# Kernel optimization log

Hardware: AMD Instinct MI355X
Metric: run time of the kernel (lower is better)

The kernel has to match this reference:

```python
import jax, jax.numpy as jnp
import numpy as np

B, N, S = 256, 512, 32
D_ENT, D_KEY, D_IN, D_FUNC, D_TYPE, H = 256, 32, 1024, 256, 259, 32


def _init_linear(k, out_d, in_d):
    kw, kb = jax.random.split(k)
    bound = 1.0 / np.sqrt(in_d)
    W = jax.random.uniform(kw, (out_d, in_d), minval=-bound, maxval=bound, dtype=jnp.float32)
    b = jax.random.uniform(kb, (out_d,), minval=-bound, maxval=bound, dtype=jnp.float32)
    return W, b


def setup_inputs() -> dict:
    key = jax.random.key(0)
    ks = jax.random.split(key, 16)
    inp = {
        "embedding": jax.random.normal(ks[0], (B, D_IN), jnp.float32),
        "available_unit_type_mask": (jax.random.uniform(ks[1], (B, D_TYPE)) < 0.5).astype(jnp.float32),
        "available_units_mask": jnp.ones((B, N), jnp.float32),
        "entity_embedding": jax.random.normal(ks[2], (B, N, D_ENT), jnp.float32),
        "selected_units": jax.random.randint(ks[3], (B, S), 0, N, dtype=jnp.int32),
        "end_embedding": jax.random.uniform(ks[4], (1, D_KEY), minval=-1.0, maxval=1.0, dtype=jnp.float32) / np.sqrt(D_KEY),
    }
    inp["W_key"], inp["b_key"] = _init_linear(ks[5], D_KEY, D_ENT)
    inp["W_func"], inp["b_func"] = _init_linear(ks[6], D_FUNC, D_TYPE)
    inp["W_fc1"], inp["b_fc1"] = _init_linear(ks[7], D_FUNC, D_IN)
    inp["W_fc2"], inp["b_fc2"] = _init_linear(ks[8], D_KEY, D_FUNC)
    inp["W_embed"], inp["b_embed"] = _init_linear(ks[9], D_IN, D_KEY)
    inp["W_ih"], inp["b_ih"] = _init_linear(ks[10], 4 * H, D_KEY)
    inp["W_hh"], inp["b_hh"] = _init_linear(ks[11], 4 * H, H)
    return inp


def reference(embedding, available_unit_type_mask, available_units_mask, entity_embedding,
              selected_units, end_embedding, W_key, b_key, W_func, b_func, W_fc1, b_fc1,
              W_fc2, b_fc2, W_embed, b_embed, W_ih, b_ih, W_hh, b_hh):
    Bv, Nv, _ = entity_embedding.shape
    Sv = selected_units.shape[1]
    # keys for each entity + end-flag embedding appended -> [B, N+1, key_dim]
    key_t = jnp.einsum('bnd,kd->bnk', entity_embedding, W_key) + b_key
    end = jnp.broadcast_to(end_embedding[None, :, :], (Bv, 1, end_embedding.shape[1]))
    pad_key = jnp.concatenate([key_t, end], axis=1)
    # mask: entities + end flag; teacher-forced selected positions forced to 1
    mask0 = jnp.concatenate([available_units_mask, jnp.ones((Bv, 1), available_units_mask.dtype)], axis=1)
    mask0 = mask0.at[jnp.arange(Bv)[:, None], selected_units].set(1.0)
    func_embed = jax.nn.relu(available_unit_type_mask @ W_func.T + b_func)
    inv_n = 1.0 / jnp.float32(Nv)  # split_entity_num = end_flag_index = num_units
    bidx = jnp.arange(Bv)
    # per-step selected index (dummy 0 on the final end-flag step) and validity
    sel_seq = jnp.concatenate([selected_units.T, jnp.zeros((1, Bv), selected_units.dtype)], axis=0)
    valid_seq = jnp.concatenate([jnp.ones((Sv, Bv), jnp.float32), jnp.zeros((1, Bv), jnp.float32)], axis=0)

    def step(carry, xs):
        emb, h, c, mask = carry
        sel, valid = xs
        # query = fc2(relu(fc1(emb) + func_embed))
        x = jax.nn.relu(emb @ W_fc1.T + b_fc1 + func_embed) @ W_fc2.T + b_fc2
        # one LSTM step
        gates = x @ W_ih.T + b_ih + h @ W_hh.T + b_hh
        i_g, f_g, g_g, o_g = jnp.split(gates, 4, axis=1)
        c = jax.nn.sigmoid(f_g) * c + jax.nn.sigmoid(i_g) * jnp.tanh(g_g)
        h = jax.nn.sigmoid(o_g) * jnp.tanh(c)
        # masked dot-product over keys -> logits [B, N+1]
        q = jnp.einsum('bk,bnk->bn', h, pad_key) - (1.0 - mask) * 1e9
        # mark selected unit unavailable for subsequent steps
        mask = mask.at[bidx, sel].set(jnp.where(valid > 0, 0.0, mask[bidx, sel]))
        # one-hot gather of selected key, averaged, fed back into embedding
        emb_sel = pad_key[bidx, sel] * inv_n
        emb = emb + (emb_sel @ W_embed.T + b_embed) * valid[:, None]
        return (emb, h, c, mask), q

    h0 = jnp.zeros((Bv, W_hh.shape[1]), jnp.float32)
    c0 = jnp.zeros_like(h0)
    (emb, _, _, _), logits = jax.lax.scan(step, (embedding, h0, c0, mask0), (sel_seq, valid_seq))
    logits = jnp.transpose(logits, (1, 0, 2))  # [B, S+1, N+1]
    return logits, emb
```

## Files before the change

### kernel.cpp

```cpp
#include <hip/hip_runtime.h>
#include <math.h>

#define BB_ 256
#define NN_ 512
#define SS_ 32
#define NP1 513
#define SP1 33
#define D_IN 1024
#define D_TYPE 259
#define INV_N (1.0f/512.0f)

typedef short s16x4 __attribute__((ext_vector_type(4)));
typedef short s16x8 __attribute__((ext_vector_type(8)));
typedef float f32x4 __attribute__((ext_vector_type(4)));

#if defined(__has_builtin)
#if __has_builtin(__builtin_amdgcn_rcpf)
#define FRCP(x) __builtin_amdgcn_rcpf(x)
#else
#define FRCP(x) (1.0f / (x))
#endif
#else
#define FRCP(x) (1.0f / (x))
#endif

__device__ __forceinline__ float fsig(float x) { return FRCP(1.0f + __expf(-x)); }
__device__ __forceinline__ float ftanh(float x) { return fmaf(-2.0f, FRCP(1.0f + __expf(2.0f * x)), 1.0f); }
__device__ __forceinline__ short f2bf(float f) {
    unsigned u = __float_as_uint(f);
    unsigned r = (u + 0x7FFFu + ((u >> 16) & 1u)) >> 16;
    return (short)r;
}
__device__ __forceinline__ float bf2f(short s) {
    unsigned u = ((unsigned)(unsigned short)s) << 16;
    return __uint_as_float(u);
}

__global__ __launch_bounds__(256) void front_kernel(
    const float* __restrict__ ent, const float* __restrict__ Wk,
    const float* __restrict__ bk, const float* __restrict__ endv,
    const float* __restrict__ Wemb, const float* __restrict__ bemb,
    const float* __restrict__ Wfc1, const float* __restrict__ emb0,
    const float* __restrict__ bfc1, const float* __restrict__ atm,
    const float* __restrict__ Wf, const float* __restrict__ bf,
    short* __restrict__ pkbf, float* __restrict__ WcombT,
    float* __restrict__ cbv, float* __restrict__ act_pre)
{
    __shared__ char u_raw[33280];
    short* a_st   = (short*)u_raw;
    float* wemb_s = (float*)(u_raw + 18688);
    float* a_lds  = (float*)u_raw;
    float* w_lds  = (float*)(u_raw + 16640);

    const int tid = threadIdx.x;
    const int bid = blockIdx.x;
    const int lane = tid & 63, w = tid >> 6;
    const int nl = lane & 15, q = lane >> 4;

    if (bid < 1024) {
        const size_t rowbase = (size_t)bid * 128;
        s16x8 bfr[8][2];
#pragma unroll
        for (int s = 0; s < 8; s++)
#pragma unroll
            for (int t = 0; t < 2; t++) {
                const float* src = Wk + (size_t)(t * 16 + nl) * 256 + s * 32 + q * 8;
                float4 v0 = *(const float4*)(src);
                float4 v1 = *(const float4*)(src + 4);
                s16x8 bv;
                bv[0] = f2bf(v0.x); bv[1] = f2bf(v0.y); bv[2] = f2bf(v0.z); bv[3] = f2bf(v0.w);
                bv[4] = f2bf(v1.x); bv[5] = f2bf(v1.y); bv[6] = f2bf(v1.z); bv[7] = f2bf(v1.w);
                bfr[s][t] = bv;
            }
        f32x4 acc[2][2];
#pragma unroll
        for (int mt = 0; mt < 2; mt++)
#pragma unroll
            for (int t = 0; t < 2; t++) acc[mt][t] = (f32x4)0.0f;

        for (int kc = 0; kc < 4; ++kc) {
            __syncthreads();
#pragma unroll
            for (int p = 0; p < 8; p++) {
                int flat = p * 256 + tid;
                int row = flat >> 4;
                int f4 = flat & 15;
                float4 v = *(const float4*)(ent + (rowbase + row) * 256 + kc * 64 + f4 * 4);
                s16x4 sv;
                sv[0] = f2bf(v.x); sv[1] = f2bf(v.y); sv[2] = f2bf(v.z); sv[3] = f2bf(v.w);
                *(s16x4*)&a_st[row * 72 + f4 * 4] = sv;
            }
            __syncthreads();
#pragma unroll
            for (int ks = 0; ks < 2; ks++) {
                const int sg = kc * 2 + ks;
#pragma unroll
                for (int mt = 0; mt < 2; mt++) {
                    s16x8 af = *(const s16x8*)&a_st[(w * 32 + mt * 16 + nl) * 72 + ks * 32 + q * 8];
#pragma unroll
                    for (int t = 0; t < 2; t++)
                        acc[mt][t] = __builtin_amdgcn_mfma_f32_16x16x32_bf16(af, bfr[sg][t], acc[mt][t], 0, 0, 0);
                }
            }
        }
        float bkv[2];
        bkv[0] = bk[nl]; bkv[1] = bk[16 + nl];
#pragma unroll
        for (int mt = 0; mt < 2; mt++)
#pragma unroll
            for (int t = 0; t < 2; t++)
#pragma unroll
                for (int r = 0; r < 4; r++) {
                    int rowg = (int)rowbase + w * 32 + mt * 16 + q * 4 + r;
                    int b = rowg >> 9, n = rowg & 511;
                    pkbf[((size_t)b * NP1 + n) * 32 + t * 16 + nl] = f2bf(acc[mt][t][r] + bkv[t]);
                }
    } else if (bid < 1026) {
        const int m0 = bid - 1024;
        f32x4 acc[2][3];
#pragma unroll
        for (int mt = 0; mt < 2; mt++)
#pragma unroll
            for (int t = 0; t < 3; t++) acc[mt][t] = (f32x4)0.0f;

        for (int kc = 0; kc < 16; ++kc) {
            __syncthreads();
#pragma unroll
            for (int p = 0; p < 8; p++) {
                int flat = p * 256 + tid;
                int row = flat >> 4;
                int f4 = flat & 15;
                float4 v = *(const float4*)(Wfc1 + (size_t)(m0 * 128 + row) * D_IN + kc * 64 + f4 * 4);
                s16x4 sv;
                sv[0] = f2bf(v.x); sv[1] = f2bf(v.y); sv[2] = f2bf(v.z); sv[3] = f2bf(v.w);
                *(s16x4*)&a_st[row * 72 + f4 * 4] = sv;
            }
            {
                int r = tid >> 2, c0 = tid & 3;
#pragma unroll
                for (int cc = 0; cc < 9; cc++) {
                    int col = c0 + cc * 4;
                    if (col < 33) {
                        float v = (col < 32) ? Wemb[(size_t)(kc * 64 + r) * 32 + col]
                                             : bemb[kc * 64 + r];
                        wemb_s[r * 33 + col] = v;
                    }
                }
            }
            __syncthreads();
#pragma unroll
            for (int ks = 0; ks < 2; ks++) {
                s16x8 bv[3];
#pragma unroll
                for (int t = 0; t < 3; t++) {
                    int n = t * 16 + nl;
#pragma unroll
                    for (int jj = 0; jj < 8; jj++) {
                        float v = (n < 33) ? wemb_s[(ks * 32 + q * 8 + jj) * 33 + n] : 0.0f;
                        bv[t][jj] = f2bf(v);
                    }
                }
#pragma unroll
                for (int mt = 0; mt < 2; mt++) {
                    s16x8 af = *(const s16x8*)&a_st[(w * 32 + mt * 16 + nl) * 72 + ks * 32 + q * 8];
#pragma unroll
                    for (int t = 0; t < 3; t++)
                        acc[mt][t] = __builtin_amdgcn_mfma_f32_16x16x32_bf16(af, bv[t], acc[mt][t], 0, 0, 0);
                }
            }
        }
#pragma unroll
        for (int mt = 0; mt < 2; mt++)
#pragma unroll
            for (int t = 0; t < 3; t++)
#pragma unroll
                for (int r = 0; r < 4; r++) {
                    int j = m0 * 128 + w * 32 + mt * 16 + q * 4 + r;
                    int n = t * 16 + nl;
                    if (n < 32) WcombT[j * 32 + n] = acc[mt][t][r];
                    else if (n == 32) cbv[j] = acc[mt][t][r];
                }
    } else if (bid == 1026) {
        const int k = tid & 31, b0 = tid >> 5;
        short evk = f2bf(endv[k]);
        for (int b = b0; b < BB_; b += 8)
            pkbf[((size_t)b * NP1 + 512) * 32 + k] = evk;
    } else {
        const int idx = bid - 1027;
        const int jt = idx & 15, bt = idx >> 4;
        const int bb = tid >> 4, jj = tid & 15;

#pragma unroll 4
        for (int r = 0; r < 16; r++) {
            a_lds[r * 260 + tid] = atm[(size_t)(bt * 16 + r) * D_TYPE + tid];
            w_lds[r * 260 + tid] = Wf[(size_t)(jt * 16 + r) * D_TYPE + tid];
            if (tid < 3) {
                a_lds[r * 260 + 256 + tid] = atm[(size_t)(bt * 16 + r) * D_TYPE + 256 + tid];
                w_lds[r * 260 + 256 + tid] = Wf[(size_t)(jt * 16 + r) * D_TYPE + 256 + tid];
            }
        }
        __syncthreads();
        float accf = 0.0f;
        {
            const float4* ap = (const float4*)&a_lds[bb * 260];
            const float4* wp = (const float4*)&w_lds[jj * 260];
#pragma unroll 8
            for (int i4 = 0; i4 < 64; i4++) {
                float4 a = ap[i4]; float4 wv = wp[i4];
                accf = fmaf(a.x, wv.x, accf); accf = fmaf(a.y, wv.y, accf);
                accf = fmaf(a.z, wv.z, accf); accf = fmaf(a.w, wv.w, accf);
            }
            for (int i = 256; i < 259; i++) accf = fmaf(a_lds[bb * 260 + i], w_lds[jj * 260 + i], accf);
        }
        float acc = 0.0f;
        for (int c = 0; c < 4; c++) {
            __syncthreads();
#pragma unroll
            for (int p = 0; p < 4; p++) {
                int l4 = p * 256 + tid;
                int r = l4 >> 6, k4 = l4 & 63;
                *(float4*)&a_lds[r * 260 + k4 * 4] =
                    *(const float4*)(emb0 + (size_t)(bt * 16 + r) * D_IN + c * 256 + k4 * 4);
                *(float4*)&w_lds[r * 260 + k4 * 4] =
                    *(const float4*)(Wfc1 + (size_t)(jt * 16 + r) * D_IN + c * 256 + k4 * 4);
            }
            __syncthreads();
#pragma unroll 8
            for (int k4 = 0; k4 < 64; k4++) {
                float4 a = *(const float4*)&a_lds[bb * 260 + k4 * 4];
                float4 wv = *(const float4*)&w_lds[jj * 260 + k4 * 4];
                acc = fmaf(a.x, wv.x, acc); acc = fmaf(a.y, wv.y, acc);
                acc = fmaf(a.z, wv.z, acc); acc = fmaf(a.w, wv.w, acc);
            }
        }
        const int b = bt * 16 + bb, j = jt * 16 + jj;
        act_pre[b * 256 + j] = acc + bfc1[j] + fmaxf(accf + bf[j], 0.0f);
    }
}

__global__ __launch_bounds__(256, 1) void back_kernel(
    const short* __restrict__ pkbf, const float* __restrict__ act_pre0,
    const int* __restrict__ sel, const float* __restrict__ avail,
    const float* __restrict__ Wfc2, const float* __restrict__ bfc2,
    const float* __restrict__ Wih, const float* __restrict__ bih,
    const float* __restrict__ bhh, const float* __restrict__ Whh,
    const float* __restrict__ WcombT, const float* __restrict__ cbv,
    const float* __restrict__ emb0, const float* __restrict__ Wemb,
    const float* __restrict__ bemb,
    float* __restrict__ logits, float* __restrict__ emb_out)
{
    __shared__ float S[19204];
    __shared__ int sel_l[SS_];
    float* rap_l  = S;
    float* red_l  = S + 8580;
    float* x_l    = S + 17028;
    float* cumE_l = S + 18084;
    float* ssel_l = S + 19140;
    float* xg_l   = S;
    float* h_all  = S + 4224;
    float* m0_l   = S + 8580;
    int*   tf_l   = (int*)(S + 9093);

    const int tid = threadIdx.x;
    const int b = blockIdx.x;
    const int lane = tid & 63, w = tid >> 6;
    const int nl = lane & 15, q = lane >> 4;

    if (tid < SS_) sel_l[tid] = sel[b * SS_ + tid];

    {
        const int k = tid & 31, sq = tid >> 5;
        const int sq4 = sq * 4;
        int s0 = sel[b * SS_ + sq4 + 0];
        int s1 = sel[b * SS_ + sq4 + 1];
        int s2 = sel[b * SS_ + sq4 + 2];
        int s3 = sel[b * SS_ + sq4 + 3];
        float v0 = bf2f(pkbf[((size_t)b * NP1 + s0) * 32 + k]) * INV_N;
        float v1 = bf2f(pkbf[((size_t)b * NP1 + s1) * 32 + k]) * INV_N;
        float v2 = bf2f(pkbf[((size_t)b * NP1 + s2) * 32 + k]) * INV_N;
        float v3 = bf2f(pkbf[((size_t)b * NP1 + s3) * 32 + k]) * INV_N;
        float p0 = v0, p1 = p0 + v1, p2 = p1 + v2, p3 = p2 + v3;
        x_l[sq * 32 + k] = p3;
        __syncthreads();
        float off = 0.0f;
        for (int p = 0; p < 8; p++) if (p < sq) off += x_l[p * 32 + k];
        cumE_l[(sq4 + 1) * 32 + k] = off + p0;
        cumE_l[(sq4 + 2) * 32 + k] = off + p1;
        cumE_l[(sq4 + 3) * 32 + k] = off + p2;
        cumE_l[(sq4 + 4) * 32 + k] = off + p3;
        if (tid < 32) cumE_l[tid] = 0.0f;
        if (sq == 7) ssel_l[k] = off + p3;
    }
    __syncthreads();

    {
        float wcr[32];
#pragma unroll
        for (int k4 = 0; k4 < 8; k4++) {
            float4 v = *(const float4*)(WcombT + (size_t)tid * 32 + k4 * 4);
            wcr[k4*4] = v.x; wcr[k4*4+1] = v.y; wcr[k4*4+2] = v.z; wcr[k4*4+3] = v.w;
        }
        const float cbr = cbv[tid];
        const float ap0v = act_pre0[b * 256 + tid];
        for (int t = 0; t < SP1; ++t) {
            float ap = fmaf((float)t, cbr, ap0v);
            const float4* ce = (const float4*)&cumE_l[t * 32];
#pragma unroll
            for (int k4 = 0; k4 < 8; k4++) {
                float4 e = ce[k4];
                ap = fmaf(e.x, wcr[k4*4], ap);   ap = fmaf(e.y, wcr[k4*4+1], ap);
                ap = fmaf(e.z, wcr[k4*4+2], ap); ap = fmaf(e.w, wcr[k4*4+3], ap);
            }
            rap_l[t * 260 + tid] = fmaxf(ap, 0.0f);
        }
    }
    __syncthreads();

    {
        const int seg = tid >> 5, i = tid & 31;
        float wfc2r[32];
#pragma unroll
        for (int i4 = 0; i4 < 8; i4++) {
            float4 v = *(const float4*)(Wfc2 + (size_t)i * 256 + seg * 32 + i4 * 4);
            wfc2r[i4*4] = v.x; wfc2r[i4*4+1] = v.y; wfc2r[i4*4+2] = v.z; wfc2r[i4*4+3] = v.w;
        }
        for (int t = 0; t < SP1; ++t) {
            float part = 0.0f;
            const float4* rp = (const float4*)&rap_l[t * 260 + seg * 32];
#pragma unroll
            for (int i4 = 0; i4 < 8; i4++) {
                float4 rv = rp[i4];
                part = fmaf(rv.x, wfc2r[i4*4], part);   part = fmaf(rv.y, wfc2r[i4*4+1], part);
                part = fmaf(rv.z, wfc2r[i4*4+2], part); part = fmaf(rv.w, wfc2r[i4*4+3], part);
            }
            red_l[t * 256 + seg * 32 + i] = part;
        }
    }
    __syncthreads();

    for (int p = 0; p < 5; p++) {
        int idx = p * 256 + tid;
        if (idx < SP1 * 32) {
            int t = idx >> 5, i = idx & 31;
            float x = bfc2[i];
#pragma unroll
            for (int s = 0; s < 8; s++) x += red_l[t * 256 + s * 32 + i];
            x_l[t * 32 + i] = x;
        }
    }
    __syncthreads();

    {
        const int g = tid & 127, half = tid >> 7;
        float wihr[32];
#pragma unroll
        for (int k4 = 0; k4 < 8; k4++) {
            float4 v = *(const float4*)(Wih + (size_t)g * 32 + k4 * 4);
            wihr[k4*4] = v.x; wihr[k4*4+1] = v.y; wihr[k4*4+2] = v.z; wihr[k4*4+3] = v.w;
        }
        const float bihg = bih[g] + bhh[g];
        for (int t = half; t < SP1; t += 2) {
            float gg = bihg;
            const float4* xp = (const float4*)&x_l[t * 32];
#pragma unroll
            for (int k4 = 0; k4 < 8; k4++) {
                float4 xv = xp[k4];
                gg = fmaf(xv.x, wihr[k4*4], gg);   gg = fmaf(xv.y, wihr[k4*4+1], gg);
                gg = fmaf(xv.z, wihr[k4*4+2], gg); gg = fmaf(xv.w, wihr[k4*4+3], gg);
            }
            xg_l[t * 128 + g] = gg;
        }
    }
    __syncthreads();

    if (tid < 64) {
        float whh0[32], whh1[32];
#pragma unroll
        for (int k4 = 0; k4 < 8; k4++) {
            float4 v0 = *(const float4*)(Whh + (size_t)tid * 32 + k4 * 4);
            float4 v1 = *(const float4*)(Whh + (size_t)(tid + 64) * 32 + k4 * 4);
            whh0[k4*4] = v0.x; whh0[k4*4+1] = v0.y; whh0[k4*4+2] = v0.z; whh0[k4*4+3] = v0.w;
            whh1[k4*4] = v1.x; whh1[k4*4+1] = v1.y; whh1[k4*4+2] = v1.z; whh1[k4*4+3] = v1.w;
        }
        float c = 0.0f, h = 0.0f;
        for (int t = 0; t < SP1; ++t) {
            float g0 = xg_l[t * 128 + tid];
            float g1 = xg_l[t * 128 + 64 + tid];
            if (t > 0) {
#pragma unroll
                for (int k = 0; k < 32; k++) {
                    float hk = __shfl(h, k);
                    g0 = fmaf(hk, whh0[k], g0);
                    g1 = fmaf(hk, whh1[k], g1);
                }
            }
            float og0 = __shfl_xor(g0, 32);
            float og1 = __shfl_xor(g1, 32);
            float ig = fsig(g0);
            float fg = fsig(og0);
            float gv = ftanh(g1);
            float og = fsig(og1);
            float cn = fg * c + ig * gv;
            float hn = og * ftanh(cn);
            if (tid < 32) {
                c = cn; h = hn;
                h_all[t * 32 + tid] = hn;
            }
        }
    } else {
        for (int n = tid - 64; n < NP1; n += 192) {
            float m = (n < NN_) ? avail[(size_t)b * NN_ + n] : 1.0f;
            int tf = 1000;
#pragma unroll 8
            for (int s = 0; s < SS_; s++) {
                int sv = sel_l[s];
                if (sv == n) { m = 1.0f; if (s < tf) tf = s; }
            }
            m0_l[n] = m; tf_l[n] = tf;
        }
    }
    __syncthreads();

    {
        s16x8 afr[3];
#pragma unroll
        for (int mt = 0; mt < 3; mt++) {
            int row = mt * 16 + nl;
            s16x8 av;
#pragma unroll
            for (int jj = 0; jj < 8; jj++) {
                float v = (row < SP1) ? h_all[row * 32 + q * 8 + jj] : 0.0f;
                av[jj] = f2bf(v);
            }
            afr[mt] = av;
        }
        for (int tt = w; tt < 33; tt += 4) {
            int n = tt * 16 + nl;
            bool nv = n < NP1;
            s16x8 bv = nv ? *(const s16x8*)(pkbf + ((size_t)b * NP1 + n) * 32 + q * 8) : (s16x8)0;
            f32x4 acc[3];
#pragma unroll
            for (int mt = 0; mt < 3; mt++)
                acc[mt] = __builtin_amdgcn_mfma_f32_16x16x32_bf16(afr[mt], bv, (f32x4)0.0f, 0, 0, 0);
            float m0v = nv ? m0_l[n] : 0.0f;
            int tfv = nv ? tf_l[n] : 0;
#pragma unroll
            for (int mt = 0; mt < 3; mt++)
#pragma unroll
                for (int r = 0; r < 4; r++) {
                    int t = mt * 16 + q * 4 + r;
                    if (t < SP1 && nv) {
                        float mv = (t <= tfv) ? m0v : 0.0f;
                        logits[((size_t)b * SP1 + t) * NP1 + n] = acc[mt][r] - (1.0f - mv) * 1e9f;
                    }
                }
        }
    }

#pragma unroll
    for (int p = 0; p < 4; p++) {
        int i = p * 256 + tid;
        float acc = emb0[(size_t)b * D_IN + i] + 32.0f * bemb[i];
        const float* wr = Wemb + (size_t)i * 32;
#pragma unroll
        for (int k4 = 0; k4 < 8; k4++) {
            float4 wv = *(const float4*)(wr + k4 * 4);
            acc = fmaf(ssel_l[k4*4+0], wv.x, acc);
            acc = fmaf(ssel_l[k4*4+1], wv.y, acc);
            acc = fmaf(ssel_l[k4*4+2], wv.z, acc);
            acc = fmaf(ssel_l[k4*4+3], wv.w, acc);
        }
        emb_out[(size_t)b * D_IN + i] = acc;
    }
}

extern "C" void kernel_launch(void* const* d_in, const int* in_sizes, int n_in,
                              void* d_out, int out_size, void* d_ws, size_t ws_size,
                              hipStream_t stream)
{
    (void)in_sizes; (void)n_in; (void)out_size; (void)ws_size;
    const float* embedding = (const float*)d_in[0];
    const float* atm       = (const float*)d_in[1];
    const float* avail     = (const float*)d_in[2];
    const float* ent       = (const float*)d_in[3];
    const int*   sel       = (const int*)  d_in[4];
    const float* endv      = (const float*)d_in[5];
    const float* Wk   = (const float*)d_in[6];
    const float* bk   = (const float*)d_in[7];
    const float* Wf   = (const float*)d_in[8];
    const float* bf   = (const float*)d_in[9];
    const float* Wfc1 = (const float*)d_in[10];
    const float* bfc1 = (const float*)d_in[11];
    const float* Wfc2 = (const float*)d_in[12];
    const float* bfc2 = (const float*)d_in[13];
    const float* Wemb = (const float*)d_in[14];
    const float* bemb = (const float*)d_in[15];
    const float* Wih  = (const float*)d_in[16];
    const float* bih  = (const float*)d_in[17];
    const float* Whh  = (const float*)d_in[18];
    const float* bhh  = (const float*)d_in[19];

    float* ws = (float*)d_ws;
    float* act_pre = ws;
    float* WcombT  = act_pre + BB_ * 256;
    float* cbv     = WcombT + 256 * 32;
    short* pkbf    = (short*)(cbv + 256);

    float* logits  = (float*)d_out;
    float* emb_out = logits + (size_t)BB_ * SP1 * NP1;

    front_kernel<<<1283, 256, 0, stream>>>(ent, Wk, bk, endv, Wemb, bemb,
                                           Wfc1, embedding, bfc1, atm, Wf, bf,
                                           pkbf, WcombT, cbv, act_pre);
    back_kernel<<<BB_, 256, 0, stream>>>(pkbf, act_pre, sel, avail,
                                         Wfc2, bfc2, Wih, bih, bhh, Whh,
                                         WcombT, cbv, embedding, Wemb, bemb,
                                         logits, emb_out);
}
```

Measured before the change: 310.6 us.

## Double-buffer entity key GEMM with async global-to-LDS loads and reorder block roles

The entity-key projection blocks now handle 64 rows each (2048 blocks) and stream fp32 entity tiles straight into LDS with global_load_lds in a double-buffered, XOR-swizzled layout, converting to bf16 at fragment-read time instead of on the store path. Block roles are reordered so the fc1/func-embed blocks and the Wcomb blocks come first in the grid, and the fp32 dot loops use four independent accumulators. The goal is to overlap global loads with MFMA work, spread the memory-bound key GEMM over more blocks, and start the long-running blocks early. In exchange it relies on hand-placed waitcnt/barrier sequencing, which is fragile, and it spends more LDS bandwidth reading fp32.

Result: faster. 298.9 us (-3.8%).

```diff
diff --git a/kernel.cpp b/kernel.cpp
--- a/kernel.cpp
+++ b/kernel.cpp
@@ -9,6 +9,13 @@
 #define D_IN 1024
 #define D_TYPE 259
 #define INV_N (1.0f/512.0f)
+
+#define N_ACT 256
+#define COMB_BASE 256
+#define END_BID 258
+#define KEY_BASE 259
+#define N_KEY 2048
+#define FRONT_GRID (KEY_BASE + N_KEY)
 
 typedef short s16x4 __attribute__((ext_vector_type(4)));
 typedef short s16x8 __attribute__((ext_vector_type(8)));
@@ -46,19 +53,39 @@
     short* __restrict__ pkbf, float* __restrict__ WcombT,
     float* __restrict__ cbv, float* __restrict__ act_pre)
 {
-    __shared__ char u_raw[33280];
+    __shared__ __align__(128) char u_raw[33280];
     short* a_st   = (short*)u_raw;
     float* wemb_s = (float*)(u_raw + 18688);
     float* a_lds  = (float*)u_raw;
     float* w_lds  = (float*)(u_raw + 16640);
+    float* kb     = (float*)u_raw;
 
     const int tid = threadIdx.x;
     const int bid = blockIdx.x;
     const int lane = tid & 63, w = tid >> 6;
     const int nl = lane & 15, q = lane >> 4;
 
-    if (bid < 1024) {
-        const size_t rowbase = (size_t)bid * 128;
+    if (bid >= KEY_BASE) {
+        const size_t rowbase = (size_t)(bid - KEY_BASE) * 64;
+
+#define KSTAGE(kc_, bi_) do {                                                     \
+        _Pragma("unroll")                                                         \
+        for (int p_ = 0; p_ < 4; p_++) {                                          \
+            int flat_ = p_ * 256 + tid;                                           \
+            int row_ = flat_ >> 4, u_ = flat_ & 15;                               \
+            int gf4_ = (u_ & 8) | ((u_ ^ row_) & 7);                              \
+            const float* src_ = ent + (((rowbase + (size_t)row_) << 8)            \
+                                       + (kc_) * 64 + gf4_ * 4);                  \
+            char* dst_ = u_raw + (bi_) * 16384 + ((p_ << 8) + (w << 6)) * 16;     \
+            __builtin_amdgcn_global_load_lds(                                     \
+                (const __attribute__((address_space(1))) void*)src_,              \
+                (__attribute__((address_space(3))) void*)dst_, 16, 0, 0);         \
+        }                                                                         \
+    } while (0)
+
+        KSTAGE(0, 0);
+        KSTAGE(1, 1);
+
         s16x8 bfr[8][2];
 #pragma unroll
         for (int s = 0; s < 8; s++)
@@ -72,51 +99,113 @@
                 bv[4] = f2bf(v1.x); bv[5] = f2bf(v1.y); bv[6] = f2bf(v1.z); bv[7] = f2bf(v1.w);
                 bfr[s][t] = bv;
             }
-        f32x4 acc[2][2];
-#pragma unroll
-        for (int mt = 0; mt < 2; mt++)
-#pragma unroll
-            for (int t = 0; t < 2; t++) acc[mt][t] = (f32x4)0.0f;
-
+
+        f32x4 acc[2];
+        acc[0] = (f32x4)0.0f; acc[1] = (f32x4)0.0f;
+
+        const int rl = w * 16 + nl;
+        const int rx = rl & 7;
+
+        asm volatile("s_waitcnt vmcnt(4)" ::: "memory");
+        __builtin_amdgcn_s_barrier();
+        asm volatile("" ::: "memory");
+
+#pragma unroll
         for (int kc = 0; kc < 4; ++kc) {
+            const float* kbc = kb + (kc & 1) * 4096;
+#pragma unroll
+            for (int ks = 0; ks < 2; ks++) {
+                int s0 = ks * 8 + ((q * 2) ^ rx);
+                int s1 = ks * 8 + ((q * 2 + 1) ^ rx);
+                f32x4 a0 = *(const f32x4*)&kbc[rl * 64 + s0 * 4];
+                f32x4 a1 = *(const f32x4*)&kbc[rl * 64 + s1 * 4];
+                s16x8 af;
+                af[0] = f2bf(a0[0]); af[1] = f2bf(a0[1]); af[2] = f2bf(a0[2]); af[3] = f2bf(a0[3]);
+                af[4] = f2bf(a1[0]); af[5] = f2bf(a1[1]); af[6] = f2bf(a1[2]); af[7] = f2bf(a1[3]);
+                acc[0] = __builtin_amdgcn_mfma_f32_16x16x32_bf16(af, bfr[kc * 2 + ks][0], acc[0], 0, 0, 0);
+                acc[1] = __builtin_amdgcn_mfma_f32_16x16x32_bf16(af, bfr[kc * 2 + ks][1], acc[1], 0, 0, 0);
+            }
+            if (kc < 2) {
+                asm volatile("s_waitcnt lgkmcnt(0)" ::: "memory");
+                __builtin_amdgcn_s_barrier();
+                asm volatile("" ::: "memory");
+                KSTAGE(kc + 2, kc & 1);
+                asm volatile("s_waitcnt vmcnt(4)" ::: "memory");
+                __builtin_amdgcn_s_barrier();
+                asm volatile("" ::: "memory");
+            } else if (kc == 2) {
+                asm volatile("s_waitcnt vmcnt(0)" ::: "memory");
+                __builtin_amdgcn_s_barrier();
+                asm volatile("" ::: "memory");
+            }
+        }
+#undef KSTAGE
+
+        float bkv0 = bk[nl], bkv1 = bk[16 + nl];
+#pragma unroll
+        for (int t = 0; t < 2; t++)
+#pragma unroll
+            for (int r = 0; r < 4; r++) {
+                int rowg = (int)rowbase + w * 16 + q * 4 + r;
+                int b = rowg >> 9, n = rowg & 511;
+                pkbf[((size_t)b * NP1 + n) * 32 + t * 16 + nl] =
+                    f2bf(acc[t][r] + (t ? bkv1 : bkv0));
+            }
+    } else if (bid < N_ACT) {
+        const int idx = bid;
+        const int jt = idx & 15, bt = idx >> 4;
+        const int bb = tid >> 4, jj = tid & 15;
+
+#pragma unroll 4
+        for (int r = 0; r < 16; r++) {
+            a_lds[r * 260 + tid] = atm[(size_t)(bt * 16 + r) * D_TYPE + tid];
+            w_lds[r * 260 + tid] = Wf[(size_t)(jt * 16 + r) * D_TYPE + tid];
+            if (tid < 3) {
+                a_lds[r * 260 + 256 + tid] = atm[(size_t)(bt * 16 + r) * D_TYPE + 256 + tid];
+                w_lds[r * 260 + 256 + tid] = Wf[(size_t)(jt * 16 + r) * D_TYPE + 256 + tid];
+            }
+        }
+        __syncthreads();
+        float accf;
+        {
+            float f0 = 0.0f, f1 = 0.0f, f2 = 0.0f, f3 = 0.0f;
+            const float4* ap = (const float4*)&a_lds[bb * 260];
+            const float4* wp = (const float4*)&w_lds[jj * 260];
+#pragma unroll 8
+            for (int i4 = 0; i4 < 64; i4++) {
+                float4 a = ap[i4]; float4 wv = wp[i4];
+                f0 = fmaf(a.x, wv.x, f0); f1 = fmaf(a.y, wv.y, f1);
+                f2 = fmaf(a.z, wv.z, f2); f3 = fmaf(a.w, wv.w, f3);
+            }
+            accf = (f0 + f1) + (f2 + f3);
+            for (int i = 256; i < 259; i++) accf = fmaf(a_lds[bb * 260 + i], w_lds[jj * 260 + i], accf);
+        }
+        float c0 = 0.0f, c1 = 0.0f, c2 = 0.0f, c3 = 0.0f;
+        for (int c = 0; c < 4; c++) {
             __syncthreads();
 #pragma unroll
-            for (int p = 0; p < 8; p++) {
-                int flat = p * 256 + tid;
-                int row = flat >> 4;
-                int f4 = flat & 15;
-                float4 v = *(const float4*)(ent + (rowbase + row) * 256 + kc * 64 + f4 * 4);
-                s16x4 sv;
-                sv[0] = f2bf(v.x); sv[1] = f2bf(v.y); sv[2] = f2bf(v.z); sv[3] = f2bf(v.w);
-                *(s16x4*)&a_st[row * 72 + f4 * 4] = sv;
+            for (int p = 0; p < 4; p++) {
+                int l4 = p * 256 + tid;
+                int r = l4 >> 6, k4 = l4 & 63;
+                *(float4*)&a_lds[r * 260 + k4 * 4] =
+                    *(const float4*)(emb0 + (size_t)(bt * 16 + r) * D_IN + c * 256 + k4 * 4);
+                *(float4*)&w_lds[r * 260 + k4 * 4] =
+                    *(const float4*)(Wfc1 + (size_t)(jt * 16 + r) * D_IN + c * 256 + k4 * 4);
             }
             __syncthreads();
-#pragma unroll
-            for (int ks = 0; ks < 2; ks++) {
-                const int sg = kc * 2 + ks;
-#pragma unroll
-                for (int mt = 0; mt < 2; mt++) {
-                    s16x8 af = *(const s16x8*)&a_st[(w * 32 + mt * 16 + nl) * 72 + ks * 32 + q * 8];
-#pragma unroll
-                    for (int t = 0; t < 2; t++)
-                        acc[mt][t] = __builtin_amdgcn_mfma_f32_16x16x32_bf16(af, bfr[sg][t], acc[mt][t], 0, 0, 0);
-                }
-            }
-        }
-        float bkv[2];
-        bkv[0] = bk[nl]; bkv[1] = bk[16 + nl];
-#pragma unroll
-        for (int mt = 0; mt < 2; mt++)
-#pragma unroll
-            for (int t = 0; t < 2; t++)
-#pragma unroll
-                for (int r = 0; r < 4; r++) {
-                    int rowg = (int)rowbase + w * 32 + mt * 16 + q * 4 + r;
-                    int b = rowg >> 9, n = rowg & 511;
-                    pkbf[((size_t)b * NP1 + n) * 32 + t * 16 + nl] = f2bf(acc[mt][t][r] + bkv[t]);
-                }
-    } else if (bid < 1026) {
-        const int m0 = bid - 1024;
+#pragma unroll 8
+            for (int k4 = 0; k4 < 64; k4++) {
+                float4 a = *(const float4*)&a_lds[bb * 260 + k4 * 4];
+                float4 wv = *(const float4*)&w_lds[jj * 260 + k4 * 4];
+                c0 = fmaf(a.x, wv.x, c0); c1 = fmaf(a.y, wv.y, c1);
+                c2 = fmaf(a.z, wv.z, c2); c3 = fmaf(a.w, wv.w, c3);
+            }
+        }
+        float acc = (c0 + c1) + (c2 + c3);
+        const int b = bt * 16 + bb, j = jt * 16 + jj;
+        act_pre[b * 256 + j] = acc + bfc1[j] + fmaxf(accf + bf[j], 0.0f);
+    } else if (bid < END_BID) {
+        const int m0 = bid - COMB_BASE;
         f32x4 acc[2][3];
 #pragma unroll
         for (int mt = 0; mt < 2; mt++)
@@ -180,61 +269,11 @@
                     if (n < 32) WcombT[j * 32 + n] = acc[mt][t][r];
                     else if (n == 32) cbv[j] = acc[mt][t][r];
                 }
-    } else if (bid == 1026) {
+    } else {
         const int k = tid & 31, b0 = tid >> 5;
         short evk = f2bf(endv[k]);
         for (int b = b0; b < BB_; b += 8)
             pkbf[((size_t)b * NP1 + 512) * 32 + k] = evk;
-    } else {
-        const int idx = bid - 1027;
-        const int jt = idx & 15, bt = idx >> 4;
-        const int bb = tid >> 4, jj = tid & 15;
-
-#pragma unroll 4
-        for (int r = 0; r < 16; r++) {
-            a_lds[r * 260 + tid] = atm[(size_t)(bt * 16 + r) * D_TYPE + tid];
-            w_lds[r * 260 + tid] = Wf[(size_t)(jt * 16 + r) * D_TYPE + tid];
-            if (tid < 3) {
-                a_lds[r * 260 + 256 + tid] = atm[(size_t)(bt * 16 + r) * D_TYPE + 256 + tid];
-                w_lds[r * 260 + 256 + tid] = Wf[(size_t)(jt * 16 + r) * D_TYPE + 256 + tid];
-            }
-        }
-        __syncthreads();
-        float accf = 0.0f;
-        {
-            const float4* ap = (const float4*)&a_lds[bb * 260];
-            const float4* wp = (const float4*)&w_lds[jj * 260];
-#pragma unroll 8
-            for (int i4 = 0; i4 < 64; i4++) {
-                float4 a = ap[i4]; float4 wv = wp[i4];
-                accf = fmaf(a.x, wv.x, accf); accf = fmaf(a.y, wv.y, accf);
-                accf = fmaf(a.z, wv.z, accf); accf = fmaf(a.w, wv.w, accf);
-            }
-            for (int i = 256; i < 259; i++) accf = fmaf(a_lds[bb * 260 + i], w_lds[jj * 260 + i], accf);
-        }
-        float acc = 0.0f;
-        for (int c = 0; c < 4; c++) {
-            __syncthreads();
-#pragma unroll
-            for (int p = 0; p < 4; p++) {
-                int l4 = p * 256 + tid;
-                int r = l4 >> 6, k4 = l4 & 63;
-                *(float4*)&a_lds[r * 260 + k4 * 4] =
-                    *(const float4*)(emb0 + (size_t)(bt * 16 + r) * D_IN + c * 256 + k4 * 4);
-                *(float4*)&w_lds[r * 260 + k4 * 4] =
-                    *(const float4*)(Wfc1 + (size_t)(jt * 16 + r) * D_IN + c * 256 + k4 * 4);
-            }
-            __syncthreads();
-#pragma unroll 8
-            for (int k4 = 0; k4 < 64; k4++) {
-                float4 a = *(const float4*)&a_lds[bb * 260 + k4 * 4];
-                float4 wv = *(const float4*)&w_lds[jj * 260 + k4 * 4];
-                acc = fmaf(a.x, wv.x, acc); acc = fmaf(a.y, wv.y, acc);
-                acc = fmaf(a.z, wv.z, acc); acc = fmaf(a.w, wv.w, acc);
-            }
-        }
-        const int b = bt * 16 + bb, j = jt * 16 + jj;
-        act_pre[b * 256 + j] = acc + bfc1[j] + fmaxf(accf + bf[j], 0.0f);
     }
 }
 
@@ -509,9 +548,9 @@
     float* logits  = (float*)d_out;
     float* emb_out = logits + (size_t)BB_ * SP1 * NP1;
 
-    front_kernel<<<1283, 256, 0, stream>>>(ent, Wk, bk, endv, Wemb, bemb,
-                                           Wfc1, embedding, bfc1, atm, Wf, bf,
-                                           pkbf, WcombT, cbv, act_pre);
+    front_kernel<<<FRONT_GRID, 256, 0, stream>>>(ent, Wk, bk, endv, Wemb, bemb,
+                                                 Wfc1, embedding, bfc1, atm, Wf, bf,
+                                                 pkbf, WcombT, cbv, act_pre);
     back_kernel<<<BB_, 256, 0, stream>>>(pkbf, act_pre, sel, avail,
                                          Wfc2, bfc2, Wih, bih, bhh, Whh,
                                          WcombT, cbv, embedding, Wemb, bemb,
```
